# Performance work log

Measured on AMD Instinct MI355X. Metric: run time of the kernel, lower is better.

## Reference

```python
import jax, jax.numpy as jnp
import numpy as np

B, S, T, D = 8, 8, 256, 256          # batch, series, time_steps, input_dim
H, DK = 8, 64                         # attn_heads, attn_dim
HD = H * DK                           # 512
L = 2                                 # attn_layers
F = 256                               # mlp_dim
R = 512                               # resolution
M = 128                               # number of mid-points sampled this step
EPS = 1e-5


def setup_inputs() -> dict:
    key = jax.random.key(0)
    ks = iter(jax.random.split(key, 64))

    def rn(shape, scale=0.05):
        return scale * jax.random.normal(next(ks), shape, dtype=jnp.float32)

    inp = {
        'encoded': jax.random.normal(next(ks), (B, S, T, D), dtype=jnp.float32),
        'true_u': jax.random.uniform(next(ks), (B, S, T), dtype=jnp.float32),
        'mid_idx': jnp.sort(jax.random.randint(next(ks), (M,), 0, T)),
        'left_idx': jax.random.randint(next(ks), (M,), 0, T),
        'right_idx': jax.random.randint(next(ks), (M,), 0, T),
        'i': 3,
        # dimension_shift
        'ds_W': rn((D, HD)), 'ds_b': jnp.zeros((HD,), jnp.float32),
        # per-layer, per-head key-creator MLPs (stacked): (D+1) -> F -> F -> DK
        'kW1': rn((L, H, D + 1, F)), 'kb1': jnp.zeros((L, H, F), jnp.float32),
        'kW2': rn((L, H, F, F)),     'kb2': jnp.zeros((L, H, F), jnp.float32),
        'kW3': rn((L, H, F, DK)),    'kb3': jnp.zeros((L, H, DK), jnp.float32),
        # value-creator MLPs
        'vW1': rn((L, H, D + 1, F)), 'vb1': jnp.zeros((L, H, F), jnp.float32),
        'vW2': rn((L, H, F, F)),     'vb2': jnp.zeros((L, H, F), jnp.float32),
        'vW3': rn((L, H, F, DK)),    'vb3': jnp.zeros((L, H, DK), jnp.float32),
        # attention / feed-forward layer norms
        'ln1_g': jnp.ones((L, HD), jnp.float32), 'ln1_b': jnp.zeros((L, HD), jnp.float32),
        'ln2_g': jnp.ones((L, HD), jnp.float32), 'ln2_b': jnp.zeros((L, HD), jnp.float32),
        # feed-forwards
        'ffW1': rn((L, HD, HD)), 'ffb1': jnp.zeros((L, HD), jnp.float32),
        'ffW2': rn((L, HD, HD)), 'ffb2': jnp.zeros((L, HD), jnp.float32),
        # dist_extractors MLP: HD -> F -> F -> R
        'deW1': rn((HD, F)), 'deb1': jnp.zeros((F,), jnp.float32),
        'deW2': rn((F, F)),  'deb2': jnp.zeros((F,), jnp.float32),
        'deW3': rn((F, R)),  'deb3': jnp.zeros((R,), jnp.float32),
    }
    return inp


def _mlp_heads(x, W1, b1, W2, b2, W3, b3):
    # x: [B,S,T,D+1]; weights: [L,H,...] -> out [L,B,S,T,H,DK]
    h = jax.nn.relu(jnp.einsum('bstc,lhcf->lbsthf', x, W1) + b1[:, None, None, None])
    h = jax.nn.relu(jnp.einsum('lbsthf,lhfg->lbsthg', h, W2) + b2[:, None, None, None])
    return jnp.einsum('lbsthg,lhgd->lbsthd', h, W3) + b3[:, None, None, None]


def _ln(x, g, b):
    mu = jnp.mean(x, axis=-1, keepdims=True)
    var = jnp.mean(jnp.square(x - mu), axis=-1, keepdims=True)
    return (x - mu) * jax.lax.rsqrt(var + EPS) * g + b


def reference(encoded, true_u, mid_idx, left_idx, right_idx, i,
              ds_W, ds_b,
              kW1, kb1, kW2, kb2, kW3, kb3,
              vW1, vb1, vW2, vb2, vW3, vb3,
              ln1_g, ln1_b, ln2_g, ln2_b,
              ffW1, ffb1, ffW2, ffb2,
              deW1, deb1, deW2, deb2, deW3, deb3):
    # merged_input = cat([encoded, true_u[..., None]])  -> [B,S,T,D+1]
    merged = jnp.concatenate([encoded, true_u[..., None]], axis=-1)

    keys = _mlp_heads(merged, kW1, kb1, kW2, kb2, kW3, kb3)   # [L,B,S,T,H,DK]
    values = _mlp_heads(merged, vW1, vb1, vW2, vb2, vW3, vb3)  # [L,B,S,T,H,DK]

    srange = jnp.arange(S)
    # n=1 neighbor: time index = loop counter m for series < i, else right[m]
    # (faithful to keys_hist[:, :i, mid:mid+1] in the original)
    idx1 = jnp.where(srange[None, :] < i, jnp.arange(M)[:, None], right_idx[:, None])  # [M,S]

    def gather_neighbors(kv):  # kv: [L,B,S,T,H,DK] -> [L,B,M,S,2,H,DK]
        n0 = jnp.transpose(kv[:, :, :, left_idx], (0, 1, 3, 2, 4, 5))  # [L,B,M,S,H,DK]
        n1 = kv[:, :, srange[None, :], idx1]                            # [L,B,M,S,H,DK]
        return jnp.stack([n0, n1], axis=4)

    nk = gather_neighbors(keys)
    nv = gather_neighbors(values)

    pred = encoded[:, i, mid_idx]                  # [B,M,D]
    att_value = pred @ ds_W + ds_b                 # [B,M,HD]

    scale = DK ** (-0.5)
    for l in range(L):
        avh = att_value.reshape(B, M, H, DK)
        prod = jnp.einsum('bmhd,bmsnhd->bmhsn', avh, nk[l]) * scale
        w = jax.nn.softmax(prod, axis=-1)          # softmax over n only, as in source
        att = jnp.einsum('bmhsn,bmsnhd->bmhd', w, nv[l]).reshape(B, M, HD)
        x = _ln(att_value + att, ln1_g[l], ln1_b[l])
        ff = jax.nn.relu(x @ ffW1[l] + ffb1[l]) @ ffW2[l] + ffb2[l]
        att_value = _ln(x + ff, ln2_g[l], ln2_b[l])

    h = jax.nn.relu(att_value @ deW1 + deb1)
    h = jax.nn.relu(h @ deW2 + deb2)
    logits = h @ deW3 + deb3                       # [B,M,R]
    return logits
```

## Files before the change

### kernel.cpp

```cpp
#include <hip/hip_runtime.h>
#include <hip/hip_bf16.h>

#define NB 8
#define NS 8
#define NT 256
#define ND 256
#define NH 8
#define NDK 64
#define NHD 512
#define NL 2
#define NF 256
#define NR 512
#define NM 128
#define NTOK 16384
#define NROW 1024

typedef __attribute__((ext_vector_type(8))) short short8;
typedef __attribute__((ext_vector_type(4))) float f32x4;

__device__ __forceinline__ unsigned short f2bf(float x) {
    unsigned u = __builtin_bit_cast(unsigned, x);
    unsigned r = (u + 0x7fffu + ((u >> 16) & 1u)) >> 16;
    return (unsigned short)r;
}
__device__ __forceinline__ float bf2f(unsigned short x) {
    return __builtin_bit_cast(float, ((unsigned)x) << 16);
}
__device__ __forceinline__ float wred(float v) {
#pragma unroll
    for (int o = 32; o > 0; o >>= 1) v += __shfl_xor(v, o, 64);
    return v;
}

__global__ __launch_bounds__(256) void prep_all(
    const float* __restrict__ enc,
    const float* __restrict__ kW1, const float* __restrict__ kW2, const float* __restrict__ kW3,
    const float* __restrict__ vW1, const float* __restrict__ vW2, const float* __restrict__ vW3,
    const float* __restrict__ dsW, const float* __restrict__ ffW1,
    const float* __restrict__ ffW2, const float* __restrict__ deW1,
    const float* __restrict__ deW2, const float* __restrict__ deW3,
    unsigned short* __restrict__ XF, unsigned short* __restrict__ WP,
    float* __restrict__ W1L, unsigned short* __restrict__ WG) {
    __shared__ float T[32][257];
    int bid = blockIdx.x, tid = threadIdx.x;
    if (bid < 512) {
        int t0 = bid * 32;
        const float* src = enc + (size_t)t0 * 256;
#pragma unroll
        for (int it = 0; it < 8; ++it) {
            int f4 = it * 256 + tid;
            int row = f4 >> 6, c = (f4 & 63) * 4;
            float4 v = *(const float4*)(src + row * 256 + c);
            T[row][c] = v.x; T[row][c + 1] = v.y; T[row][c + 2] = v.z; T[row][c + 3] = v.w;
        }
        __syncthreads();
        int tile = t0 >> 7, g = (t0 >> 6) & 1, nt0 = (t0 >> 4) & 3;
#pragma unroll
        for (int i = 0; i < 32; i += 8) {
            int o = tid * 32 + i;
            int lane = (o >> 3) & 63, ntp = (o >> 9) & 1, kc = o >> 10;
            int id = lane & 15, quad = lane >> 4;
            __align__(16) unsigned short p[8];
#pragma unroll
            for (int j = 0; j < 8; ++j) p[j] = f2bf(T[ntp * 16 + id][kc * 32 + quad * 8 + j]);
            size_t dsto = ((size_t)((((tile * 8 + kc) * 2 + g) * 4 + (nt0 + ntp)) * 64 + lane)) * 8;
            *(uint4*)(XF + dsto) = *(uint4*)p;
        }
    } else if (bid < 1280) {
        int lb = bid - 512;
        int combo = lb / 24, r = lb % 24;
        int st = r >> 3, kc = r & 7;
        int kvv = combo >> 4, l = (combo >> 3) & 1, h = combo & 7;
        unsigned short* dstc = WP + (size_t)combo * 147456;
        if (st < 2) {
            const float* W = (st == 0) ? (kvv ? vW1 : kW1) : (kvv ? vW2 : kW2);
            int rows = (st == 0) ? 257 : 256;
            const float* src = W + ((size_t)(l * 8 + h) * rows + kc * 32) * 256;
#pragma unroll
            for (int it = 0; it < 8; ++it) {
                int f4 = it * 256 + tid;
                int row = f4 >> 6, c = (f4 & 63) * 4;
                float4 v = *(const float4*)(src + (size_t)row * 256 + c);
                T[row][c] = v.x; T[row][c + 1] = v.y; T[row][c + 2] = v.z; T[row][c + 3] = v.w;
            }
            __syncthreads();
            unsigned short* dst = dstc + st * 65536 + kc * 8192;
#pragma unroll
            for (int i = 0; i < 32; i += 8) {
                int o = tid * 32 + i;
                int lane = (o >> 3) & 63, ftile = o >> 9;
                int id = lane & 15, quad = lane >> 4;
                __align__(16) unsigned short p[8];
#pragma unroll
                for (int j = 0; j < 8; ++j) p[j] = f2bf(T[quad * 8 + j][ftile * 16 + id]);
                *(uint4*)(dst + o) = *(uint4*)p;
            }
            if (st == 0 && kc == 0) {
                const float* hw = (kvv ? vW1 : kW1) + (size_t)(l * 8 + h) * 257 * 256;
                W1L[combo * 256 + tid] = hw[65536 + tid];
            }
        } else {
            const float* src = (kvv ? vW3 : kW3) + ((size_t)(l * 8 + h) * 256 + kc * 32) * 64;
#pragma unroll
            for (int it = 0; it < 2; ++it) {
                int f4 = it * 256 + tid;
                int row = f4 >> 4, c = (f4 & 15) * 4;
                float4 v = *(const float4*)(src + (size_t)row * 64 + c);
                T[row][c] = v.x; T[row][c + 1] = v.y; T[row][c + 2] = v.z; T[row][c + 3] = v.w;
            }
            __syncthreads();
            unsigned short* dst = dstc + 131072 + kc * 2048;
            int o = tid * 8;
            int lane = tid & 63, ftile = tid >> 6;
            int id = lane & 15, quad = lane >> 4;
            __align__(16) unsigned short p[8];
#pragma unroll
            for (int j = 0; j < 8; ++j) p[j] = f2bf(T[quad * 8 + j][ftile * 16 + id]);
            *(uint4*)(dst + o) = *(uint4*)p;
        }
    } else {
        int lb0 = bid - 1280;
        const float* src; int N, kc, ng; size_t base;
        if (lb0 < 32)       { int lb = lb0;       src = dsW;           N = 512; base = 0;       kc = lb >> 2; ng = lb & 3; }
        else if (lb0 < 96)  { int lb = lb0 - 32;  src = ffW1;          N = 512; base = 131072;  kc = lb >> 2; ng = lb & 3; }
        else if (lb0 < 160) { int lb = lb0 - 96;  src = ffW1 + 262144; N = 512; base = 393216;  kc = lb >> 2; ng = lb & 3; }
        else if (lb0 < 224) { int lb = lb0 - 160; src = ffW2;          N = 512; base = 655360;  kc = lb >> 2; ng = lb & 3; }
        else if (lb0 < 288) { int lb = lb0 - 224; src = ffW2 + 262144; N = 512; base = 917504;  kc = lb >> 2; ng = lb & 3; }
        else if (lb0 < 320) { int lb = lb0 - 288; src = deW1;          N = 256; base = 1179648; kc = lb >> 1; ng = lb & 1; }
        else if (lb0 < 336) { int lb = lb0 - 320; src = deW2;          N = 256; base = 1310720; kc = lb >> 1; ng = lb & 1; }
        else                { int lb = lb0 - 336; src = deW3;          N = 512; base = 1376256; kc = lb >> 2; ng = lb & 3; }
        int NTl = N >> 4;
        const float* s = src + (size_t)(kc * 32) * N + ng * 128;
#pragma unroll
        for (int it = 0; it < 4; ++it) {
            int f4 = it * 256 + tid;
            int row = f4 >> 5, c = (f4 & 31) * 4;
            float4 v = *(const float4*)(s + (size_t)row * N + c);
            T[row][c] = v.x; T[row][c + 1] = v.y; T[row][c + 2] = v.z; T[row][c + 3] = v.w;
        }
        __syncthreads();
        unsigned short* d = WG + base + (size_t)(kc * NTl + ng * 8) * 512;
#pragma unroll
        for (int i = 0; i < 16; i += 8) {
            int o = tid * 16 + i;
            int lane = (o >> 3) & 63, ntl = o >> 9;
            int id = lane & 15, quad = lane >> 4;
            __align__(16) unsigned short p[8];
#pragma unroll
            for (int j = 0; j < 8; ++j) p[j] = f2bf(T[quad * 8 + j][ntl * 16 + id]);
            *(uint4*)(d + o) = *(uint4*)p;
        }
    }
}

__global__ __launch_bounds__(256, 4) void heads_mlp(
    const float* __restrict__ tu, const unsigned short* __restrict__ XF,
    const unsigned short* __restrict__ WP, const float* __restrict__ W1L,
    const float* __restrict__ kb1, const float* __restrict__ kb2, const float* __restrict__ kb3,
    const float* __restrict__ vb1, const float* __restrict__ vb2, const float* __restrict__ vb3,
    unsigned short* __restrict__ KV) {
    __shared__ __align__(16) unsigned short smem[16896];

    const int tid = threadIdx.x;
    const int w2 = tid >> 6, lane = tid & 63, id = lane & 15, quad = lane >> 4;
    const int combo = blockIdx.x & 31, t64 = blockIdx.x >> 5;
    const int kvv = combo >> 4, l = (combo >> 3) & 1, h = combo & 7;
    const int r0 = t64 * 64;
    const int tile128 = t64 >> 1, g = t64 & 1;
    const unsigned short* WF1 = WP + (size_t)combo * 147456;
    const unsigned short* WF2 = WF1 + 65536;
    const unsigned short* WF3 = WF1 + 131072;
    const float* b1 = (kvv ? vb1 : kb1) + (l * 8 + h) * 256;
    const float* b2 = (kvv ? vb2 : kb2) + (l * 8 + h) * 256;
    const float* b3 = (kvv ? vb3 : kb3) + (l * 8 + h) * 64;

    {
        const uint4* s = (const uint4*)(XF + (size_t)tile128 * 32768 + g * 2048);
        uint4* d = (uint4*)smem;
#pragma unroll
        for (int kc = 0; kc < 8; ++kc) d[kc * 256 + tid] = s[kc * 512 + tid];
    }
    __syncthreads();

    f32x4 acc[4][4];
#pragma unroll
    for (int i = 0; i < 4; ++i)
#pragma unroll
        for (int j = 0; j < 4; ++j) acc[i][j] = (f32x4){0.f, 0.f, 0.f, 0.f};

    {
        short8 af[4], afn[4];
#pragma unroll
        for (int ft = 0; ft < 4; ++ft)
            af[ft] = *(const short8*)(WF1 + (size_t)((w2 * 4 + ft) * 64 + lane) * 8);
#pragma unroll
        for (int kc = 0; kc < 8; ++kc) {
            if (kc < 7) {
#pragma unroll
                for (int ft = 0; ft < 4; ++ft)
                    afn[ft] = *(const short8*)(WF1 + (size_t)(((kc + 1) * 16 + w2 * 4 + ft) * 64 + lane) * 8);
            }
            short8 bf[4];
#pragma unroll
            for (int nt = 0; nt < 4; ++nt)
                bf[nt] = *(const short8*)(smem + (size_t)(kc * 4 + nt) * 512 + lane * 8);
#pragma unroll
            for (int ft = 0; ft < 4; ++ft)
#pragma unroll
                for (int nt = 0; nt < 4; ++nt)
                    acc[ft][nt] = __builtin_amdgcn_mfma_f32_16x16x32_bf16(af[ft], bf[nt], acc[ft][nt], 0, 0, 0);
#pragma unroll
            for (int ft = 0; ft < 4; ++ft) af[ft] = afn[ft];
        }
    }
    __syncthreads();
    {
        float ur[4];
#pragma unroll
        for (int nt = 0; nt < 4; ++nt) ur[nt] = tu[r0 + nt * 16 + id];
#pragma unroll
        for (int ft = 0; ft < 4; ++ft) {
            int fb = w2 * 64 + ft * 16 + quad * 4;
            float4 bb = *(const float4*)(b1 + fb);
            float4 wl = *(const float4*)(W1L + combo * 256 + fb);
            const float* bbp = (const float*)&bb;
            const float* wlp = (const float*)&wl;
#pragma unroll
            for (int nt = 0; nt < 4; ++nt) {
                unsigned short p[4];
#pragma unroll
                for (int r = 0; r < 4; ++r) {
                    float v = acc[ft][nt][r] + bbp[r] + ur[nt] * wlp[r];
                    p[r] = f2bf(fmaxf(v, 0.f));
                }
                uint2 pk;
                pk.x = (unsigned)p[0] | ((unsigned)p[1] << 16);
                pk.y = (unsigned)p[2] | ((unsigned)p[3] << 16);
                *(uint2*)(smem + (size_t)(nt * 16 + id) * 264 + fb) = pk;
            }
        }
    }
    __syncthreads();

#pragma unroll
    for (int i = 0; i < 4; ++i)
#pragma unroll
        for (int j = 0; j < 4; ++j) acc[i][j] = (f32x4){0.f, 0.f, 0.f, 0.f};
    {
        short8 af[4], afn[4];
#pragma unroll
        for (int ft = 0; ft < 4; ++ft)
            af[ft] = *(const short8*)(WF2 + (size_t)((w2 * 4 + ft) * 64 + lane) * 8);
#pragma unroll
        for (int kc = 0; kc < 8; ++kc) {
            if (kc < 7) {
#pragma unroll
                for (int ft = 0; ft < 4; ++ft)
                    afn[ft] = *(const short8*)(WF2 + (size_t)(((kc + 1) * 16 + w2 * 4 + ft) * 64 + lane) * 8);
            }
            short8 bf[4];
#pragma unroll
            for (int nt = 0; nt < 4; ++nt)
                bf[nt] = *(const short8*)(smem + (size_t)(nt * 16 + id) * 264 + kc * 32 + quad * 8);
#pragma unroll
            for (int ft = 0; ft < 4; ++ft)
#pragma unroll
                for (int nt = 0; nt < 4; ++nt)
                    acc[ft][nt] = __builtin_amdgcn_mfma_f32_16x16x32_bf16(af[ft], bf[nt], acc[ft][nt], 0, 0, 0);
#pragma unroll
            for (int ft = 0; ft < 4; ++ft) af[ft] = afn[ft];
        }
    }
    __syncthreads();
#pragma unroll
    for (int ft = 0; ft < 4; ++ft) {
        int fb = w2 * 64 + ft * 16 + quad * 4;
        float4 bb = *(const float4*)(b2 + fb);
        const float* bbp = (const float*)&bb;
#pragma unroll
        for (int nt = 0; nt < 4; ++nt) {
            unsigned short p[4];
#pragma unroll
            for (int r = 0; r < 4; ++r)
                p[r] = f2bf(fmaxf(acc[ft][nt][r] + bbp[r], 0.f));
            uint2 pk;
            pk.x = (unsigned)p[0] | ((unsigned)p[1] << 16);
            pk.y = (unsigned)p[2] | ((unsigned)p[3] << 16);
            *(uint2*)(smem + (size_t)(nt * 16 + id) * 264 + fb) = pk;
        }
    }
    __syncthreads();

    f32x4 a3[4];
#pragma unroll
    for (int i = 0; i < 4; ++i) a3[i] = (f32x4){0.f, 0.f, 0.f, 0.f};
    {
        short8 af3[4], af3n[4];
#pragma unroll
        for (int ft = 0; ft < 4; ++ft)
            af3[ft] = *(const short8*)(WF3 + (size_t)(ft * 64 + lane) * 8);
#pragma unroll
        for (int kc = 0; kc < 8; ++kc) {
            if (kc < 7) {
#pragma unroll
                for (int ft = 0; ft < 4; ++ft)
                    af3n[ft] = *(const short8*)(WF3 + (size_t)(((kc + 1) * 4 + ft) * 64 + lane) * 8);
            }
            short8 b3f = *(const short8*)(smem + (size_t)(w2 * 16 + id) * 264 + kc * 32 + quad * 8);
#pragma unroll
            for (int ft = 0; ft < 4; ++ft)
                a3[ft] = __builtin_amdgcn_mfma_f32_16x16x32_bf16(af3[ft], b3f, a3[ft], 0, 0, 0);
#pragma unroll
            for (int ft = 0; ft < 4; ++ft) af3[ft] = af3n[ft];
        }
    }
    __syncthreads();
    {
        int tl = w2 * 16 + id;
#pragma unroll
        for (int ft = 0; ft < 4; ++ft) {
            int dk0 = ft * 16 + quad * 4;
            float4 bb = *(const float4*)(b3 + dk0);
            const float* bbp = (const float*)&bb;
            unsigned short p[4];
#pragma unroll
            for (int r = 0; r < 4; ++r) p[r] = f2bf(a3[ft][r] + bbp[r]);
            uint2 pk;
            pk.x = (unsigned)p[0] | ((unsigned)p[1] << 16);
            pk.y = (unsigned)p[2] | ((unsigned)p[3] << 16);
            *(uint2*)(smem + (size_t)tl * 72 + dk0) = pk;
        }
    }
    __syncthreads();
    {
#pragma unroll
        for (int it = 0; it < 2; ++it) {
            int tl = it * 32 + (tid >> 3), part = tid & 7;
            uint4 v = *(const uint4*)(smem + (size_t)tl * 72 + part * 8);
            size_t base = ((size_t)((l * 2 + kvv) * NTOK + r0 + tl)) * 512 + h * 64 + part * 8;
            *(uint4*)(KV + base) = v;
        }
    }
}

__global__ __launch_bounds__(256) void gemm_ds(
    const float* __restrict__ enc, const int* __restrict__ mid,
    const int* __restrict__ ip, const unsigned short* __restrict__ WF,
    const float* __restrict__ bias, float* __restrict__ outf) {
    int tid = threadIdx.x, wv = tid >> 6, lane = tid & 63;
    int id = lane & 15, quad = lane >> 4;
    int ntile = blockIdx.x * 4 + wv;
    int n0 = ntile * 16, m0 = blockIdx.y * 32;
    int iv = ip[0];
    int r0 = m0 + id, r1 = m0 + 16 + id;
    const float* a0p = enc + (((size_t)((r0 >> 7) * 8 + iv)) * 256 + mid[r0 & 127]) * 256 + quad * 8;
    const float* a1p = enc + (((size_t)((r1 >> 7) * 8 + iv)) * 256 + mid[r1 & 127]) * 256 + quad * 8;
    f32x4 acc[2];
    acc[0] = (f32x4){0.f, 0.f, 0.f, 0.f};
    acc[1] = (f32x4){0.f, 0.f, 0.f, 0.f};
#pragma unroll
    for (int kc = 0; kc < 8; ++kc) {
        short8 bw = *(const short8*)(WF + (size_t)((kc * 32 + ntile) * 64 + lane) * 8);
        float4 u0 = *(const float4*)(a0p + kc * 32);
        float4 u1 = *(const float4*)(a0p + kc * 32 + 4);
        float4 w0 = *(const float4*)(a1p + kc * 32);
        float4 w1 = *(const float4*)(a1p + kc * 32 + 4);
        short8 a0, a1;
        a0[0] = (short)f2bf(u0.x); a0[1] = (short)f2bf(u0.y); a0[2] = (short)f2bf(u0.z); a0[3] = (short)f2bf(u0.w);
        a0[4] = (short)f2bf(u1.x); a0[5] = (short)f2bf(u1.y); a0[6] = (short)f2bf(u1.z); a0[7] = (short)f2bf(u1.w);
        a1[0] = (short)f2bf(w0.x); a1[1] = (short)f2bf(w0.y); a1[2] = (short)f2bf(w0.z); a1[3] = (short)f2bf(w0.w);
        a1[4] = (short)f2bf(w1.x); a1[5] = (short)f2bf(w1.y); a1[6] = (short)f2bf(w1.z); a1[7] = (short)f2bf(w1.w);
        acc[0] = __builtin_amdgcn_mfma_f32_16x16x32_bf16(a0, bw, acc[0], 0, 0, 0);
        acc[1] = __builtin_amdgcn_mfma_f32_16x16x32_bf16(a1, bw, acc[1], 0, 0, 0);
    }
    float bv = bias[n0 + id];
#pragma unroll
    for (int mt = 0; mt < 2; ++mt) {
#pragma unroll
        for (int r = 0; r < 4; ++r) {
            int row = m0 + mt * 16 + quad * 4 + r;
            outf[(size_t)row * 512 + n0 + id] = acc[mt][r] + bv;
        }
    }
}

__global__ __launch_bounds__(256) void gemm_bf16(
    const unsigned short* __restrict__ A, const unsigned short* __restrict__ WF,
    const float* __restrict__ bias, const float* __restrict__ res,
    float* __restrict__ outf, unsigned short* __restrict__ outb,
    int K, int N, int relu) {
    int tid = threadIdx.x, wv = tid >> 6, lane = tid & 63;
    int id = lane & 15, quad = lane >> 4;
    int ntile = blockIdx.x * 4 + wv;
    int n0 = ntile * 16, m0 = blockIdx.y * 32;
    int NTl = N >> 4, KC = K >> 5;
    f32x4 acc[2];
    acc[0] = (f32x4){0.f, 0.f, 0.f, 0.f};
    acc[1] = (f32x4){0.f, 0.f, 0.f, 0.f};
    short8 bw = *(const short8*)(WF + (size_t)(ntile * 64 + lane) * 8);
    short8 a0 = *(const short8*)(A + (size_t)(m0 + id) * K + quad * 8);
    short8 a1 = *(const short8*)(A + (size_t)(m0 + 16 + id) * K + quad * 8);
    for (int kc = 0; kc < KC; ++kc) {
        short8 bwn, a0n, a1n;
        if (kc + 1 < KC) {
            bwn = *(const short8*)(WF + (size_t)(((kc + 1) * NTl + ntile) * 64 + lane) * 8);
            a0n = *(const short8*)(A + (size_t)(m0 + id) * K + (kc + 1) * 32 + quad * 8);
            a1n = *(const short8*)(A + (size_t)(m0 + 16 + id) * K + (kc + 1) * 32 + quad * 8);
        }
        acc[0] = __builtin_amdgcn_mfma_f32_16x16x32_bf16(a0, bw, acc[0], 0, 0, 0);
        acc[1] = __builtin_amdgcn_mfma_f32_16x16x32_bf16(a1, bw, acc[1], 0, 0, 0);
        bw = bwn; a0 = a0n; a1 = a1n;
    }
    float bv = bias[n0 + id];
#pragma unroll
    for (int mt = 0; mt < 2; ++mt) {
#pragma unroll
        for (int r = 0; r < 4; ++r) {
            int row = m0 + mt * 16 + quad * 4 + r;
            int n = n0 + id;
            float v = acc[mt][r] + bv;
            if (res) v += res[(size_t)row * N + n];
            if (relu) v = fmaxf(v, 0.f);
            if (outf) outf[(size_t)row * N + n] = v;
            if (outb) outb[(size_t)row * N + n] = f2bf(v);
        }
    }
}

__global__ __launch_bounds__(256) void attn_ln(
    const float* __restrict__ attv, const unsigned short* __restrict__ keys,
    const unsigned short* __restrict__ vals, const int* __restrict__ left,
    const int* __restrict__ right, const int* __restrict__ ip,
    const float* __restrict__ g, const float* __restrict__ bb,
    float* __restrict__ xout, unsigned short* __restrict__ xoutb) {
    int tid = threadIdx.x, wv = tid >> 6, lane = tid & 63;
    int gid = blockIdx.x * 4 + wv;
    int b = gid >> 7, m = gid & 127;
    int iv = ip[0];
    int lt = left[m], rt = right[m];
    float av8[8], att8[8];
    {
        const float* avp = attv + (size_t)gid * 512 + lane * 8;
        float4 u0 = *(const float4*)(avp);
        float4 u1 = *(const float4*)(avp + 4);
        av8[0] = u0.x; av8[1] = u0.y; av8[2] = u0.z; av8[3] = u0.w;
        av8[4] = u1.x; av8[5] = u1.y; av8[6] = u1.z; av8[7] = u1.w;
    }
#pragma unroll
    for (int j = 0; j < 8; ++j) att8[j] = 0.f;
    for (int s = 0; s < 8; ++s) {
        int t1 = (s < iv) ? m : rt;
        size_t row0 = ((size_t)((b * 8 + s) * 256 + lt)) * 512 + lane * 8;
        size_t row1 = ((size_t)((b * 8 + s) * 256 + t1)) * 512 + lane * 8;
        uint4 k0u = *(const uint4*)(keys + row0);
        uint4 k1u = *(const uint4*)(keys + row1);
        uint4 v0u = *(const uint4*)(vals + row0);
        uint4 v1u = *(const uint4*)(vals + row1);
        const unsigned short* k0 = (const unsigned short*)&k0u;
        const unsigned short* k1 = (const unsigned short*)&k1u;
        const unsigned short* v0 = (const unsigned short*)&v0u;
        const unsigned short* v1 = (const unsigned short*)&v1u;
        float p0 = 0.f, p1 = 0.f;
#pragma unroll
        for (int j = 0; j < 8; ++j) {
            p0 += av8[j] * bf2f(k0[j]);
            p1 += av8[j] * bf2f(k1[j]);
        }
#pragma unroll
        for (int o = 1; o < 8; o <<= 1) {
            p0 += __shfl_xor(p0, o, 64);
            p1 += __shfl_xor(p1, o, 64);
        }
        p0 *= 0.125f; p1 *= 0.125f;
        float mx = fmaxf(p0, p1);
        float e0 = __expf(p0 - mx), e1 = __expf(p1 - mx);
        float inv = 1.f / (e0 + e1);
        float w0 = e0 * inv, w1 = e1 * inv;
#pragma unroll
        for (int j = 0; j < 8; ++j)
            att8[j] += w0 * bf2f(v0[j]) + w1 * bf2f(v1[j]);
    }
    float x8[8], sum = 0.f;
#pragma unroll
    for (int j = 0; j < 8; ++j) { x8[j] = av8[j] + att8[j]; sum += x8[j]; }
    float mu = wred(sum) * (1.f / 512.f);
    float s2 = 0.f;
#pragma unroll
    for (int j = 0; j < 8; ++j) { float d = x8[j] - mu; s2 += d * d; }
    float rs = rsqrtf(wred(s2) * (1.f / 512.f) + 1e-5f);
    {
        const float* gp = g + lane * 8;
        const float* bp = bb + lane * 8;
        float* of = xout + (size_t)gid * 512 + lane * 8;
        unsigned short* ob = xoutb + (size_t)gid * 512 + lane * 8;
        __align__(16) float vout[8];
        __align__(16) unsigned short pb[8];
#pragma unroll
        for (int j = 0; j < 8; ++j) {
            float v = (x8[j] - mu) * rs * gp[j] + bp[j];
            vout[j] = v; pb[j] = f2bf(v);
        }
        *(float4*)(of) = *(float4*)vout;
        *(float4*)(of + 4) = *(float4*)(vout + 4);
        *(uint4*)(ob) = *(uint4*)pb;
    }
}

__global__ __launch_bounds__(256) void ln_k(const float* __restrict__ in,
                                            const float* __restrict__ g,
                                            const float* __restrict__ bb,
                                            float* __restrict__ out,
                                            unsigned short* __restrict__ outb) {
    int tid = threadIdx.x, wv = tid >> 6, lane = tid & 63;
    int gid = blockIdx.x * 4 + wv;
    float x8[8], sum = 0.f;
    {
        const float* ip = in + (size_t)gid * 512 + lane * 8;
        float4 u0 = *(const float4*)(ip);
        float4 u1 = *(const float4*)(ip + 4);
        x8[0] = u0.x; x8[1] = u0.y; x8[2] = u0.z; x8[3] = u0.w;
        x8[4] = u1.x; x8[5] = u1.y; x8[6] = u1.z; x8[7] = u1.w;
    }
#pragma unroll
    for (int j = 0; j < 8; ++j) sum += x8[j];
    float mu = wred(sum) * (1.f / 512.f);
    float s2 = 0.f;
#pragma unroll
    for (int j = 0; j < 8; ++j) { float d = x8[j] - mu; s2 += d * d; }
    float rs = rsqrtf(wred(s2) * (1.f / 512.f) + 1e-5f);
    {
        const float* gp = g + lane * 8;
        const float* bp = bb + lane * 8;
        float* of = out + (size_t)gid * 512 + lane * 8;
        unsigned short* ob = outb + (size_t)gid * 512 + lane * 8;
        __align__(16) float vout[8];
        __align__(16) unsigned short pb[8];
#pragma unroll
        for (int j = 0; j < 8; ++j) {
            float v = (x8[j] - mu) * rs * gp[j] + bp[j];
            vout[j] = v; pb[j] = f2bf(v);
        }
        *(float4*)(of) = *(float4*)vout;
        *(float4*)(of + 4) = *(float4*)(vout + 4);
        *(uint4*)(ob) = *(uint4*)pb;
    }
}

extern "C" void kernel_launch(void* const* d_in, const int* in_sizes, int n_in,
                              void* d_out, int out_size, void* d_ws, size_t ws_size,
                              hipStream_t stream) {
    const float* encoded = (const float*)d_in[0];
    const float* true_u  = (const float*)d_in[1];
    const int* mid_idx   = (const int*)d_in[2];
    const int* left_idx  = (const int*)d_in[3];
    const int* right_idx = (const int*)d_in[4];
    const int* ip        = (const int*)d_in[5];
    const float* ds_W = (const float*)d_in[6];
    const float* ds_b = (const float*)d_in[7];
    const float* kW1 = (const float*)d_in[8];
    const float* kb1 = (const float*)d_in[9];
    const float* kW2 = (const float*)d_in[10];
    const float* kb2 = (const float*)d_in[11];
    const float* kW3 = (const float*)d_in[12];
    const float* kb3 = (const float*)d_in[13];
    const float* vW1 = (const float*)d_in[14];
    const float* vb1 = (const float*)d_in[15];
    const float* vW2 = (const float*)d_in[16];
    const float* vb2 = (const float*)d_in[17];
    const float* vW3 = (const float*)d_in[18];
    const float* vb3 = (const float*)d_in[19];
    const float* ln1_g = (const float*)d_in[20];
    const float* ln1_b = (const float*)d_in[21];
    const float* ln2_g = (const float*)d_in[22];
    const float* ln2_b = (const float*)d_in[23];
    const float* ffW1 = (const float*)d_in[24];
    const float* ffb1 = (const float*)d_in[25];
    const float* ffW2 = (const float*)d_in[26];
    const float* ffb2 = (const float*)d_in[27];
    const float* deW1 = (const float*)d_in[28];
    const float* deb1 = (const float*)d_in[29];
    const float* deW2 = (const float*)d_in[30];
    const float* deb2 = (const float*)d_in[31];
    const float* deW3 = (const float*)d_in[32];
    const float* deb3 = (const float*)d_in[33];

    char* ws = (char*)d_ws;
    unsigned short* XF   = (unsigned short*)(ws + 0);
    unsigned short* WP   = (unsigned short*)(ws + 8388608);
    float* W1L           = (float*)(ws + 17825792);
    unsigned short* KV   = (unsigned short*)(ws + 17858560);
    unsigned short* WG   = (unsigned short*)(ws + 84967424);
    float* ATTV          = (float*)(ws + 87982080);
    float* XBUF          = (float*)(ws + 90079232);
    float* YBUF          = (float*)(ws + 92176384);
    unsigned short* ATTVB = (unsigned short*)(ws + 94797824);
    unsigned short* XBUFB = (unsigned short*)(ws + 95846400);
    unsigned short* FBUFB = (unsigned short*)(ws + 96894976);
    unsigned short* DE1B = XBUFB;
    unsigned short* DE2B = FBUFB;

    unsigned short* WGds  = WG + 0;
    unsigned short* WGff1_0 = WG + 131072;
    unsigned short* WGff1_1 = WG + 393216;
    unsigned short* WGff2_0 = WG + 655360;
    unsigned short* WGff2_1 = WG + 917504;
    unsigned short* WGde1 = WG + 1179648;
    unsigned short* WGde2 = WG + 1310720;
    unsigned short* WGde3 = WG + 1376256;

    prep_all<<<1648, 256, 0, stream>>>(encoded, kW1, kW2, kW3, vW1, vW2, vW3,
                                       ds_W, ffW1, ffW2, deW1, deW2, deW3,
                                       XF, WP, W1L, WG);
    heads_mlp<<<8192, 256, 0, stream>>>(true_u, XF, WP, W1L, kb1, kb2, kb3,
                                        vb1, vb2, vb3, KV);
    gemm_ds<<<dim3(8, 32), 256, 0, stream>>>(encoded, mid_idx, ip, WGds, ds_b, ATTV);
    for (int l = 0; l < 2; ++l) {
        const unsigned short* keys = KV + (size_t)(l * 2) * NTOK * NHD;
        const unsigned short* vals = KV + (size_t)(l * 2 + 1) * NTOK * NHD;
        attn_ln<<<256, 256, 0, stream>>>(ATTV, keys, vals, left_idx, right_idx, ip,
                                         ln1_g + l * 512, ln1_b + l * 512, XBUF, XBUFB);
        gemm_bf16<<<dim3(8, 32), 256, 0, stream>>>(XBUFB, (l ? WGff1_1 : WGff1_0),
                                                   ffb1 + l * 512, nullptr,
                                                   nullptr, FBUFB, 512, 512, 1);
        gemm_bf16<<<dim3(8, 32), 256, 0, stream>>>(FBUFB, (l ? WGff2_1 : WGff2_0),
                                                   ffb2 + l * 512, XBUF,
                                                   YBUF, nullptr, 512, 512, 0);
        ln_k<<<256, 256, 0, stream>>>(YBUF, ln2_g + l * 512, ln2_b + l * 512, ATTV, ATTVB);
    }
    gemm_bf16<<<dim3(4, 32), 256, 0, stream>>>(ATTVB, WGde1, deb1, nullptr,
                                               nullptr, DE1B, 512, 256, 1);
    gemm_bf16<<<dim3(4, 32), 256, 0, stream>>>(DE1B, WGde2, deb2, nullptr,
                                               nullptr, DE2B, 256, 256, 1);
    gemm_bf16<<<dim3(8, 32), 256, 0, stream>>>(DE2B, WGde3, deb3, nullptr,
                                               (float*)d_out, nullptr, 256, 512, 0);
}
```

Measured before the change: 431.0 us.

## Store K/V per head-contiguous and deepen weight-fragment prefetch in heads MLP

```diff
diff --git a/kernel.cpp b/kernel.cpp
--- a/kernel.cpp
+++ b/kernel.cpp
@@ -174,6 +174,12 @@
     const float* b2 = (kvv ? vb2 : kb2) + (l * 8 + h) * 256;
     const float* b3 = (kvv ? vb3 : kb3) + (l * 8 + h) * 64;
 
+    short8 afb[2][4];
+#pragma unroll
+    for (int ft = 0; ft < 4; ++ft) {
+        afb[0][ft] = *(const short8*)(WF1 + (size_t)((w2 * 4 + ft) * 64 + lane) * 8);
+        afb[1][ft] = *(const short8*)(WF1 + (size_t)((16 + w2 * 4 + ft) * 64 + lane) * 8);
+    }
     {
         const uint4* s = (const uint4*)(XF + (size_t)tile128 * 32768 + g * 2048);
         uint4* d = (uint4*)smem;
@@ -189,16 +195,13 @@
         for (int j = 0; j < 4; ++j) acc[i][j] = (f32x4){0.f, 0.f, 0.f, 0.f};
 
     {
-        short8 af[4], afn[4];
-#pragma unroll
-        for (int ft = 0; ft < 4; ++ft)
-            af[ft] = *(const short8*)(WF1 + (size_t)((w2 * 4 + ft) * 64 + lane) * 8);
 #pragma unroll
         for (int kc = 0; kc < 8; ++kc) {
-            if (kc < 7) {
+            short8 tn[4];
+            if (kc + 2 < 8) {
 #pragma unroll
                 for (int ft = 0; ft < 4; ++ft)
-                    afn[ft] = *(const short8*)(WF1 + (size_t)(((kc + 1) * 16 + w2 * 4 + ft) * 64 + lane) * 8);
+                    tn[ft] = *(const short8*)(WF1 + (size_t)(((kc + 2) * 16 + w2 * 4 + ft) * 64 + lane) * 8);
             }
             short8 bf[4];
 #pragma unroll
@@ -208,9 +211,11 @@
             for (int ft = 0; ft < 4; ++ft)
 #pragma unroll
                 for (int nt = 0; nt < 4; ++nt)
-                    acc[ft][nt] = __builtin_amdgcn_mfma_f32_16x16x32_bf16(af[ft], bf[nt], acc[ft][nt], 0, 0, 0);
-#pragma unroll
-            for (int ft = 0; ft < 4; ++ft) af[ft] = afn[ft];
+                    acc[ft][nt] = __builtin_amdgcn_mfma_f32_16x16x32_bf16(afb[kc & 1][ft], bf[nt], acc[ft][nt], 0, 0, 0);
+            if (kc + 2 < 8) {
+#pragma unroll
+                for (int ft = 0; ft < 4; ++ft) afb[kc & 1][ft] = tn[ft];
+            }
         }
     }
     __syncthreads();
@@ -247,16 +252,18 @@
 #pragma unroll
         for (int j = 0; j < 4; ++j) acc[i][j] = (f32x4){0.f, 0.f, 0.f, 0.f};
     {
-        short8 af[4], afn[4];
-#pragma unroll
-        for (int ft = 0; ft < 4; ++ft)
-            af[ft] = *(const short8*)(WF2 + (size_t)((w2 * 4 + ft) * 64 + lane) * 8);
+#pragma unroll
+        for (int ft = 0; ft < 4; ++ft) {
+            afb[0][ft] = *(const short8*)(WF2 + (size_t)((w2 * 4 + ft) * 64 + lane) * 8);
+            afb[1][ft] = *(const short8*)(WF2 + (size_t)((16 + w2 * 4 + ft) * 64 + lane) * 8);
+        }
 #pragma unroll
         for (int kc = 0; kc < 8; ++kc) {
-            if (kc < 7) {
+            short8 tn[4];
+            if (kc + 2 < 8) {
 #pragma unroll
                 for (int ft = 0; ft < 4; ++ft)
-                    afn[ft] = *(const short8*)(WF2 + (size_t)(((kc + 1) * 16 + w2 * 4 + ft) * 64 + lane) * 8);
+                    tn[ft] = *(const short8*)(WF2 + (size_t)(((kc + 2) * 16 + w2 * 4 + ft) * 64 + lane) * 8);
             }
             short8 bf[4];
 #pragma unroll
@@ -266,9 +273,11 @@
             for (int ft = 0; ft < 4; ++ft)
 #pragma unroll
                 for (int nt = 0; nt < 4; ++nt)
-                    acc[ft][nt] = __builtin_amdgcn_mfma_f32_16x16x32_bf16(af[ft], bf[nt], acc[ft][nt], 0, 0, 0);
-#pragma unroll
-            for (int ft = 0; ft < 4; ++ft) af[ft] = afn[ft];
+                    acc[ft][nt] = __builtin_amdgcn_mfma_f32_16x16x32_bf16(afb[kc & 1][ft], bf[nt], acc[ft][nt], 0, 0, 0);
+            if (kc + 2 < 8) {
+#pragma unroll
+                for (int ft = 0; ft < 4; ++ft) afb[kc & 1][ft] = tn[ft];
+            }
         }
     }
     __syncthreads();
@@ -337,7 +346,7 @@
         for (int it = 0; it < 2; ++it) {
             int tl = it * 32 + (tid >> 3), part = tid & 7;
             uint4 v = *(const uint4*)(smem + (size_t)tl * 72 + part * 8);
-            size_t base = ((size_t)((l * 2 + kvv) * NTOK + r0 + tl)) * 512 + h * 64 + part * 8;
+            size_t base = ((size_t)combo << 20) + (size_t)(r0 + tl) * 64 + part * 8;
             *(uint4*)(KV + base) = v;
         }
     }
@@ -428,16 +437,19 @@
 }
 
 __global__ __launch_bounds__(256) void attn_ln(
-    const float* __restrict__ attv, const unsigned short* __restrict__ keys,
-    const unsigned short* __restrict__ vals, const int* __restrict__ left,
-    const int* __restrict__ right, const int* __restrict__ ip,
+    const float* __restrict__ attv, const unsigned short* __restrict__ KV,
+    const int* __restrict__ left, const int* __restrict__ right,
+    const int* __restrict__ ip,
     const float* __restrict__ g, const float* __restrict__ bb,
-    float* __restrict__ xout, unsigned short* __restrict__ xoutb) {
+    float* __restrict__ xout, unsigned short* __restrict__ xoutb, int l) {
     int tid = threadIdx.x, wv = tid >> 6, lane = tid & 63;
     int gid = blockIdx.x * 4 + wv;
     int b = gid >> 7, m = gid & 127;
     int iv = ip[0];
     int lt = left[m], rt = right[m];
+    int h = lane >> 3, d8 = lane & 7;
+    const unsigned short* kb = KV + ((size_t)(l * 8 + h) << 20);
+    const unsigned short* vb = KV + ((size_t)(16 + l * 8 + h) << 20);
     float av8[8], att8[8];
     {
         const float* avp = attv + (size_t)gid * 512 + lane * 8;
@@ -448,14 +460,15 @@
     }
 #pragma unroll
     for (int j = 0; j < 8; ++j) att8[j] = 0.f;
+#pragma unroll 2
     for (int s = 0; s < 8; ++s) {
         int t1 = (s < iv) ? m : rt;
-        size_t row0 = ((size_t)((b * 8 + s) * 256 + lt)) * 512 + lane * 8;
-        size_t row1 = ((size_t)((b * 8 + s) * 256 + t1)) * 512 + lane * 8;
-        uint4 k0u = *(const uint4*)(keys + row0);
-        uint4 k1u = *(const uint4*)(keys + row1);
-        uint4 v0u = *(const uint4*)(vals + row0);
-        uint4 v1u = *(const uint4*)(vals + row1);
+        size_t o0 = (size_t)((b * 8 + s) * 256 + lt) * 64 + d8 * 8;
+        size_t o1 = (size_t)((b * 8 + s) * 256 + t1) * 64 + d8 * 8;
+        uint4 k0u = *(const uint4*)(kb + o0);
+        uint4 k1u = *(const uint4*)(kb + o1);
+        uint4 v0u = *(const uint4*)(vb + o0);
+        uint4 v1u = *(const uint4*)(vb + o1);
         const unsigned short* k0 = (const unsigned short*)&k0u;
         const unsigned short* k1 = (const unsigned short*)&k1u;
         const unsigned short* v0 = (const unsigned short*)&v0u;
@@ -585,28 +598,28 @@
     const float* deb3 = (const float*)d_in[33];
 
     char* ws = (char*)d_ws;
-    unsigned short* XF   = (unsigned short*)(ws + 0);
-    unsigned short* WP   = (unsigned short*)(ws + 8388608);
-    float* W1L           = (float*)(ws + 17825792);
-    unsigned short* KV   = (unsigned short*)(ws + 17858560);
-    unsigned short* WG   = (unsigned short*)(ws + 84967424);
-    float* ATTV          = (float*)(ws + 87982080);
-    float* XBUF          = (float*)(ws + 90079232);
-    float* YBUF          = (float*)(ws + 92176384);
-    unsigned short* ATTVB = (unsigned short*)(ws + 94797824);
-    unsigned short* XBUFB = (unsigned short*)(ws + 95846400);
-    unsigned short* FBUFB = (unsigned short*)(ws + 96894976);
+    unsigned short* XF    = (unsigned short*)(ws + 0);
+    unsigned short* WP    = (unsigned short*)(ws + 8388608);
+    float* W1L            = (float*)(ws + 17825792);
+    unsigned short* KV    = (unsigned short*)(ws + 17858560);
+    unsigned short* WG    = (unsigned short*)(ws + 84967424);
+    float* ATTV           = (float*)(ws + 87982080);
+    float* XBUF           = (float*)(ws + 90079232);
+    float* YBUF           = (float*)(ws + 92176384);
+    unsigned short* ATTVB = (unsigned short*)(ws + 94273536);
+    unsigned short* XBUFB = (unsigned short*)(ws + 95322112);
+    unsigned short* FBUFB = (unsigned short*)(ws + 96370688);
     unsigned short* DE1B = XBUFB;
     unsigned short* DE2B = FBUFB;
 
-    unsigned short* WGds  = WG + 0;
+    unsigned short* WGds    = WG + 0;
     unsigned short* WGff1_0 = WG + 131072;
     unsigned short* WGff1_1 = WG + 393216;
     unsigned short* WGff2_0 = WG + 655360;
     unsigned short* WGff2_1 = WG + 917504;
-    unsigned short* WGde1 = WG + 1179648;
-    unsigned short* WGde2 = WG + 1310720;
-    unsigned short* WGde3 = WG + 1376256;
+    unsigned short* WGde1   = WG + 1179648;
+    unsigned short* WGde2   = WG + 1310720;
+    unsigned short* WGde3   = WG + 1376256;
 
     prep_all<<<1648, 256, 0, stream>>>(encoded, kW1, kW2, kW3, vW1, vW2, vW3,
                                        ds_W, ffW1, ffW2, deW1, deW2, deW3,
@@ -615,10 +628,9 @@
                                         vb1, vb2, vb3, KV);
     gemm_ds<<<dim3(8, 32), 256, 0, stream>>>(encoded, mid_idx, ip, WGds, ds_b, ATTV);
     for (int l = 0; l < 2; ++l) {
-        const unsigned short* keys = KV + (size_t)(l * 2) * NTOK * NHD;
-        const unsigned short* vals = KV + (size_t)(l * 2 + 1) * NTOK * NHD;
-        attn_ln<<<256, 256, 0, stream>>>(ATTV, keys, vals, left_idx, right_idx, ip,
-                                         ln1_g + l * 512, ln1_b + l * 512, XBUF, XBUFB);
+        attn_ln<<<256, 256, 0, stream>>>(ATTV, KV, left_idx, right_idx, ip,
+                                         ln1_g + l * 512, ln1_b + l * 512,
+                                         XBUF, XBUFB, l);
         gemm_bf16<<<dim3(8, 32), 256, 0, stream>>>(XBUFB, (l ? WGff1_1 : WGff1_0),
                                                    ffb1 + l * 512, nullptr,
                                                    nullptr, FBUFB, 512, 512, 1);
```

Measured after the change: 440.1 us. 1.02x slower.
